# Optimization experiments

Measured on AMD Instinct MI355X. Metric: run time of the kernel, lower is better.

Reference implementation:

```python
import jax, jax.numpy as jnp
import numpy as np

CLAMP = 60.0
EPS = 1e-4

def _make_weights(N, alpha_logits, delta_logits, beta_logits):
    alpha = jax.nn.sigmoid(alpha_logits)   # [C,H]
    delta = jax.nn.sigmoid(delta_logits)
    beta = jax.nn.sigmoid(beta_logits)
    A = alpha * beta                        # [C,H]
    r = jnp.clip(1.0 - alpha * delta, EPS, 1.0 - EPS)
    t = jnp.arange(N, dtype=jnp.float32)[:, None, None]   # [N,1,1]
    logr = jnp.clip(jnp.log(r) * t, -CLAMP, CLAMP)        # [N,C,H]
    return A, jnp.exp(logr), jnp.exp(-logr)

def _ema_fwd(x, A, eta, r_pos, r_neg):
    # x: [B,N,C] -> y: [B,N,C]
    z = A * x[..., None] * r_neg            # [B,N,C,H]
    h = jnp.cumsum(z, axis=1) * r_pos       # [B,N,C,H]
    return jnp.sum(eta * h, axis=-1)        # [B,N,C]

def reference(x, alpha_logits, delta_logits, beta_logits, eta, proj_w, proj_b):
    B, N, C = x.shape
    A, r_pos, r_neg = _make_weights(N, alpha_logits, delta_logits, beta_logits)
    xf = x.astype(jnp.float32)
    y_fwd = _ema_fwd(xf, A, eta, r_pos, r_neg)
    y_bwd = _ema_fwd(xf[:, ::-1], A, eta, r_pos, r_neg)[:, ::-1]
    z = jnp.concatenate([y_fwd, y_bwd], axis=-1).astype(x.dtype)  # [B,N,2C]
    return z @ proj_w.T + proj_b            # [B,N,C]

def setup_inputs():
    key = jax.random.key(0)
    ks = jax.random.split(key, 7)
    B, N, C, H = 8, 4096, 512, 4
    return {
        "x": jax.random.normal(ks[0], (B, N, C), dtype=jnp.float32),
        "alpha_logits": jax.random.normal(ks[1], (C, H), dtype=jnp.float32),
        "delta_logits": jax.random.normal(ks[2], (C, H), dtype=jnp.float32),
        "beta_logits": jax.random.normal(ks[3], (C, H), dtype=jnp.float32),
        "eta": jax.random.normal(ks[4], (C, H), dtype=jnp.float32) * 0.02,
        "proj_w": jax.random.normal(ks[5], (C, 2 * C), dtype=jnp.float32) / np.sqrt(2.0 * C),
        "proj_b": jax.random.normal(ks[6], (C,), dtype=jnp.float32) * 0.01,
    }
```

## Files before the change

kernel.cpp:

```cpp
#include <hip/hip_runtime.h>
#include <hip/hip_bf16.h>

#define B_ 8
#define N_ 4096
#define C_ 512
#define H_ 4
#define EPS_ 1e-4f
#define E60P 1.14200739e26f
#define E60M 8.7565108e-27f

typedef __attribute__((ext_vector_type(8))) short short8;
typedef __attribute__((ext_vector_type(4))) float floatx4;
typedef __attribute__((ext_vector_type(2))) float floatx2;
typedef __attribute__((ext_vector_type(4))) unsigned short ushort4_t;
typedef unsigned short ushort_t;

__device__ __forceinline__ float sigmoidf_(float v) {
    return 1.0f / (1.0f + expf(-v));
}

__device__ __forceinline__ int pk_off(int t, int w, int k0, int ks, int f,
                                      int lane8, int kb) {
    return ((((t * 2 + w) * 16 + k0) * 2 + ks) * 4 + f) * 512 + lane8 * 8 + kb;
}

__device__ __forceinline__ void gload16(const void* g, void* l) {
    __builtin_amdgcn_global_load_lds(
        (const __attribute__((address_space(1))) void*)g,
        (__attribute__((address_space(3))) void*)l, 16, 0, 0);
}

__global__ __launch_bounds__(256) void k_partials3(
    const float* __restrict__ x, const float* __restrict__ al,
    const float* __restrict__ dl, const float* __restrict__ bl,
    float* __restrict__ P)
{
    int bid   = blockIdx.x;
    int chunk = bid & 15;
    int ct    = (bid >> 4) & 7;
    int b     = bid >> 7;
    int lane  = threadIdx.x & 63;
    int wave  = threadIdx.x >> 6;
    int c     = ct * 64 + lane;
    int sub   = chunk * 4 + wave;
    int t0f   = sub * 64;
    int t0b   = (63 - sub) * 64;

    float aa[4], dd[4], bb[4];
    { float4 v = ((const float4*)al)[c]; aa[0]=v.x; aa[1]=v.y; aa[2]=v.z; aa[3]=v.w; }
    { float4 v = ((const float4*)dl)[c]; dd[0]=v.x; dd[1]=v.y; dd[2]=v.z; dd[3]=v.w; }
    { float4 v = ((const float4*)bl)[c]; bb[0]=v.x; bb[1]=v.y; bb[2]=v.z; bb[3]=v.w; }

    float A[H_], ri[H_], Lh[H_];
    #pragma unroll
    for (int h = 0; h < H_; ++h) {
        float alpha = sigmoidf_(aa[h]);
        float delta = sigmoidf_(dd[h]);
        float beta  = sigmoidf_(bb[h]);
        A[h] = alpha * beta;
        float r = fminf(fmaxf(1.0f - alpha * delta, EPS_), 1.0f - EPS_);
        Lh[h] = logf(r);
        ri[h] = 1.0f / r;
    }
    const floatx2 E2P = {E60P, E60P};
    floatx2 A2[2]  = {{A[0],  A[1]},  {A[2],  A[3]}};
    floatx2 ri2[2] = {{ri[0], ri[1]}, {ri[2], ri[3]}};

    const float* xp = x + ((size_t)b * N_ + t0f) * C_ + c;

    floatx2 ep2[2], T2[2];
    #pragma unroll
    for (int p = 0; p < 2; ++p) {
        ep2[p] = (floatx2){expf(fminf(-Lh[2*p]   * (float)t0f, 60.0f)),
                           expf(fminf(-Lh[2*p+1] * (float)t0f, 60.0f))};
        T2[p]  = (floatx2){0.f, 0.f};
    }
    {
        float cur[8];
        #pragma unroll
        for (int j = 0; j < 8; ++j) cur[j] = xp[(size_t)j * C_];
        #pragma unroll 1
        for (int g = 0; g < 8; ++g) {
            float nxt[8];
            if (g < 7) {
                #pragma unroll
                for (int j = 0; j < 8; ++j)
                    nxt[j] = xp[(size_t)(g * 8 + 8 + j) * C_];
            }
            #pragma unroll
            for (int j = 0; j < 8; ++j) {
                floatx2 xv2 = {cur[j], cur[j]};
                #pragma unroll
                for (int p = 0; p < 2; ++p) {
                    T2[p] += (A2[p] * xv2) * ep2[p];
                    ep2[p] = __builtin_elementwise_min(ep2[p] * ri2[p], E2P);
                }
            }
            if (g < 7) {
                #pragma unroll
                for (int j = 0; j < 8; ++j) cur[j] = nxt[j];
            }
        }
        float* pp = P + ((size_t)b * 64 + sub) * (H_ * C_) + c;
        pp[0]      = T2[0].x;  pp[C_]     = T2[0].y;
        pp[2 * C_] = T2[1].x;  pp[3 * C_] = T2[1].y;
    }

    #pragma unroll
    for (int p = 0; p < 2; ++p) {
        ep2[p] = (floatx2){expf(fminf(-Lh[2*p]   * (float)t0b, 60.0f)),
                           expf(fminf(-Lh[2*p+1] * (float)t0b, 60.0f))};
        T2[p]  = (floatx2){0.f, 0.f};
    }
    {
        float cur[8];
        #pragma unroll
        for (int j = 0; j < 8; ++j) cur[j] = xp[(size_t)(63 - j) * C_];
        #pragma unroll 1
        for (int g = 0; g < 8; ++g) {
            float nxt[8];
            if (g < 7) {
                #pragma unroll
                for (int j = 0; j < 8; ++j)
                    nxt[j] = xp[(size_t)(63 - (g * 8 + 8 + j)) * C_];
            }
            #pragma unroll
            for (int j = 0; j < 8; ++j) {
                floatx2 xv2 = {cur[j], cur[j]};
                #pragma unroll
                for (int p = 0; p < 2; ++p) {
                    T2[p] += (A2[p] * xv2) * ep2[p];
                    ep2[p] = __builtin_elementwise_min(ep2[p] * ri2[p], E2P);
                }
            }
            if (g < 7) {
                #pragma unroll
                for (int j = 0; j < 8; ++j) cur[j] = nxt[j];
            }
        }
        float* pp = P + ((size_t)(8 + b) * 64 + (63 - sub)) * (H_ * C_) + c;
        pp[0]      = T2[0].x;  pp[C_]     = T2[0].y;
        pp[2 * C_] = T2[1].x;  pp[3 * C_] = T2[1].y;
    }
}

__global__ __launch_bounds__(256) void k_scan(float* __restrict__ P)
{
    int bid = blockIdx.x;
    int ct  = bid & 7;
    int b   = (bid >> 3) & 7;
    int dir = bid >> 6;
    int cl  = threadIdx.x & 63;
    int h   = threadIdx.x >> 6;
    int c   = ct * 64 + cl;

    float* base = P + ((size_t)(dir * 8 + b) * 64) * (H_ * C_) + h * C_ + c;

    float v[64];
    #pragma unroll
    for (int s = 0; s < 64; ++s) v[s] = base[s * (H_ * C_)];

    float run = 0.0f;
    #pragma unroll
    for (int s = 0; s < 64; ++s) { float t = v[s]; v[s] = run; run += t; }

    #pragma unroll
    for (int s = 0; s < 64; ++s) base[s * (H_ * C_)] = v[s];
}

__global__ __launch_bounds__(256) void k_apply3(
    const float* __restrict__ x, const float* __restrict__ al,
    const float* __restrict__ dl, const float* __restrict__ bl,
    const float* __restrict__ eta, const float* __restrict__ P,
    ushort_t* __restrict__ Zp)
{
    int bid   = blockIdx.x;
    int chunk = bid & 15;
    int ct    = (bid >> 4) & 7;
    int b     = bid >> 7;
    int lane  = threadIdx.x & 63;
    int wave  = threadIdx.x >> 6;
    int c     = ct * 64 + lane;
    int sub   = chunk * 4 + wave;
    int t0f   = sub * 64;
    int t0b   = (63 - sub) * 64;

    int ksv = lane >> 5, qv = (lane >> 3) & 3, kbv = lane & 7;
    int mt  = b * 32 + (t0f >> 7);
    int wq  = (t0f >> 6) & 1;
    int offcF = pk_off(mt, wq, ct,     ksv, 0, qv * 16, kbv);
    int offcB = pk_off(mt, wq, 8 + ct, ksv, 0, qv * 16, kbv);

    float aa[4], dd[4], bb[4], ee[4];
    { float4 v = ((const float4*)al )[c]; aa[0]=v.x; aa[1]=v.y; aa[2]=v.z; aa[3]=v.w; }
    { float4 v = ((const float4*)dl )[c]; dd[0]=v.x; dd[1]=v.y; dd[2]=v.z; dd[3]=v.w; }
    { float4 v = ((const float4*)bl )[c]; bb[0]=v.x; bb[1]=v.y; bb[2]=v.z; bb[3]=v.w; }
    { float4 v = ((const float4*)eta)[c]; ee[0]=v.x; ee[1]=v.y; ee[2]=v.z; ee[3]=v.w; }

    float A[H_], rr[H_], ri[H_], Lh[H_];
    #pragma unroll
    for (int h = 0; h < H_; ++h) {
        float alpha = sigmoidf_(aa[h]);
        float delta = sigmoidf_(dd[h]);
        float beta  = sigmoidf_(bb[h]);
        A[h] = alpha * beta;
        float r = fminf(fmaxf(1.0f - alpha * delta, EPS_), 1.0f - EPS_);
        Lh[h] = logf(r);
        rr[h] = r;
        ri[h] = 1.0f / r;
    }
    const floatx2 E2P = {E60P, E60P};
    const floatx2 E2M = {E60M, E60M};
    floatx2 A2[2]  = {{A[0],  A[1]},  {A[2],  A[3]}};
    floatx2 ri2[2] = {{ri[0], ri[1]}, {ri[2], ri[3]}};
    floatx2 rr2[2] = {{rr[0], rr[1]}, {rr[2], rr[3]}};
    floatx2 ee2[2] = {{ee[0], ee[1]}, {ee[2], ee[3]}};

    const float* xp = x + ((size_t)b * N_ + t0f) * C_ + c;

    {
        const float* cp = P + ((size_t)b * 64 + sub) * (H_ * C_) + c;
        floatx2 ep2[2], em2[2], S2[2];
        #pragma unroll
        for (int p = 0; p < 2; ++p) {
            ep2[p] = (floatx2){expf(fminf(-Lh[2*p]   * (float)t0f, 60.0f)),
                               expf(fminf(-Lh[2*p+1] * (float)t0f, 60.0f))};
            em2[p] = (floatx2){expf(fmaxf( Lh[2*p]   * (float)t0f, -60.0f)),
                               expf(fmaxf( Lh[2*p+1] * (float)t0f, -60.0f))};
            S2[p]  = (floatx2){cp[(2*p) * C_], cp[(2*p+1) * C_]};
        }
        float cur[8];
        #pragma unroll
        for (int j = 0; j < 8; ++j) cur[j] = xp[(size_t)j * C_];
        #pragma unroll 1
        for (int g = 0; g < 8; ++g) {
            float nxt[8];
            if (g < 7) {
                #pragma unroll
                for (int j = 0; j < 8; ++j)
                    nxt[j] = xp[(size_t)(g * 8 + 8 + j) * C_];
            }
            #pragma unroll
            for (int j = 0; j < 8; ++j) {
                int i = g * 8 + j;
                floatx2 xv2 = {cur[j], cur[j]};
                floatx2 acc = {0.f, 0.f};
                #pragma unroll
                for (int p = 0; p < 2; ++p) {
                    S2[p] += (A2[p] * xv2) * ep2[p];
                    ep2[p] = __builtin_elementwise_min(ep2[p] * ri2[p], E2P);
                    acc   += ee2[p] * (em2[p] * S2[p]);
                    em2[p] = __builtin_elementwise_max(em2[p] * rr2[p], E2M);
                }
                float y = acc.x + acc.y;
                __hip_bfloat16 yb = __float2bfloat16(y);
                Zp[offcF + (i >> 4) * 512 + (i & 15) * 8] = *(ushort_t*)&yb;
            }
            if (g < 7) {
                #pragma unroll
                for (int j = 0; j < 8; ++j) cur[j] = nxt[j];
            }
        }
    }

    {
        const float* cp = P + ((size_t)(8 + b) * 64 + (63 - sub)) * (H_ * C_) + c;
        floatx2 ep2[2], em2[2], S2[2];
        #pragma unroll
        for (int p = 0; p < 2; ++p) {
            ep2[p] = (floatx2){expf(fminf(-Lh[2*p]   * (float)t0b, 60.0f)),
                               expf(fminf(-Lh[2*p+1] * (float)t0b, 60.0f))};
            em2[p] = (floatx2){expf(fmaxf( Lh[2*p]   * (float)t0b, -60.0f)),
                               expf(fmaxf( Lh[2*p+1] * (float)t0b, -60.0f))};
            S2[p]  = (floatx2){cp[(2*p) * C_], cp[(2*p+1) * C_]};
        }
        float cur[8];
        #pragma unroll
        for (int j = 0; j < 8; ++j) cur[j] = xp[(size_t)(63 - j) * C_];
        #pragma unroll 1
        for (int g = 0; g < 8; ++g) {
            float nxt[8];
            if (g < 7) {
                #pragma unroll
                for (int j = 0; j < 8; ++j)
                    nxt[j] = xp[(size_t)(63 - (g * 8 + 8 + j)) * C_];
            }
            #pragma unroll
            for (int j = 0; j < 8; ++j) {
                int i = 63 - (g * 8 + j);
                floatx2 xv2 = {cur[j], cur[j]};
                floatx2 acc = {0.f, 0.f};
                #pragma unroll
                for (int p = 0; p < 2; ++p) {
                    S2[p] += (A2[p] * xv2) * ep2[p];
                    ep2[p] = __builtin_elementwise_min(ep2[p] * ri2[p], E2P);
                    acc   += ee2[p] * (em2[p] * S2[p]);
                    em2[p] = __builtin_elementwise_max(em2[p] * rr2[p], E2M);
                }
                float y = acc.x + acc.y;
                __hip_bfloat16 yb = __float2bfloat16(y);
                Zp[offcB + (i >> 4) * 512 + (i & 15) * 8] = *(ushort_t*)&yb;
            }
            if (g < 7) {
                #pragma unroll
                for (int j = 0; j < 8; ++j) cur[j] = nxt[j];
            }
        }
    }
}

__global__ __launch_bounds__(256) void k_cvtw2(const float* __restrict__ w,
                                               ushort_t* __restrict__ Wp)
{
    int i4 = blockIdx.x * 256 + threadIdx.x;
    int i  = i4 << 2;
    int n = i >> 10, k = i & 1023;
    int nt = n >> 7, rn = n & 127;
    int k0 = k >> 6, kk = k & 63;
    int off = pk_off(nt, rn >> 6, k0, kk >> 5, (rn >> 4) & 3,
                     ((kk >> 3) & 3) * 16 + (rn & 15), kk & 7);
    float4 v = ((const float4*)w)[i4];
    ushort4_t r;
    { __hip_bfloat16 t = __float2bfloat16(v.x); r.x = *(ushort_t*)&t; }
    { __hip_bfloat16 t = __float2bfloat16(v.y); r.y = *(ushort_t*)&t; }
    { __hip_bfloat16 t = __float2bfloat16(v.z); r.z = *(ushort_t*)&t; }
    { __hip_bfloat16 t = __float2bfloat16(v.w); r.w = *(ushort_t*)&t; }
    *(ushort4_t*)&Wp[off] = r;
}

__global__ __launch_bounds__(256, 4) void k_gemm3(
    const ushort_t* __restrict__ Zp, const ushort_t* __restrict__ Wp,
    const float* __restrict__ bias, float* __restrict__ out)
{
    __shared__ __align__(16) char lds[32768];
    char*  ldsA = lds;
    char*  ldsB = lds + 16384;
    float* stg  = (float*)lds;

    int tid  = threadIdx.x;
    int lane = tid & 63, wave = tid >> 6;
    int wm   = wave & 1, wn = wave >> 1;
    int fr   = lane & 15, quad = lane >> 4;

    int bid = blockIdx.x;
    int mt  = ((bid >> 5) << 3) | (bid & 7);
    int nt  = (bid >> 3) & 3;
    int m0  = mt * 128, n0 = nt * 128;

    const ushort_t* Az = Zp + ((size_t)(mt * 2) * 16) * 4096;
    const ushort_t* Bz = Wp + ((size_t)(nt * 2) * 16) * 4096;

    floatx4 acc[4][4];
    #pragma unroll
    for (int mf = 0; mf < 4; ++mf)
        #pragma unroll
        for (int nf = 0; nf < 4; ++nf)
            acc[mf][nf] = (floatx4){0.f, 0.f, 0.f, 0.f};

    for (int k0 = 0; k0 < 16; ++k0) {
        const ushort_t* As = Az + (size_t)k0 * 4096;
        const ushort_t* Bs = Bz + (size_t)k0 * 4096;
        #pragma unroll
        for (int w = 0; w < 2; ++w)
            #pragma unroll
            for (int inst = 0; inst < 2; ++inst) {
                gload16(As + w * 65536 + inst * 2048 + tid * 8,
                        ldsA + w * 8192 + inst * 4096 + tid * 16);
                gload16(Bs + w * 65536 + inst * 2048 + tid * 8,
                        ldsB + w * 8192 + inst * 4096 + tid * 16);
            }
        asm volatile("s_waitcnt vmcnt(0)" ::: "memory");
        __syncthreads();

        #pragma unroll
        for (int ks = 0; ks < 2; ++ks) {
            short8 af[4], bf[4];
            #pragma unroll
            for (int f = 0; f < 4; ++f) {
                af[f] = *(const short8*)(ldsA + wm * 8192 + (ks * 4 + f) * 1024 + lane * 16);
                bf[f] = *(const short8*)(ldsB + wn * 8192 + (ks * 4 + f) * 1024 + lane * 16);
            }
            #pragma unroll
            for (int mf = 0; mf < 4; ++mf)
                #pragma unroll
                for (int nf = 0; nf < 4; ++nf)
                    acc[mf][nf] = __builtin_amdgcn_mfma_f32_16x16x32_bf16(
                        af[mf], bf[nf], acc[mf][nf], 0, 0, 0);
        }
        __syncthreads();
    }

    int rrow = tid >> 3;
    int seg  = tid & 7;
    int gcol = n0 + seg * 16;

    #pragma unroll
    for (int ch = 0; ch < 4; ++ch) {
        if ((wave & 1) == (ch >> 1)) {
            int ml = (ch & 1) * 2;
            #pragma unroll
            for (int mi = 0; mi < 2; ++mi) {
                #pragma unroll
                for (int nf = 0; nf < 4; ++nf) {
                    int col = wn * 64 + nf * 16 + fr;
                    #pragma unroll
                    for (int rg = 0; rg < 4; ++rg) {
                        int row = mi * 16 + quad * 4 + rg;
                        stg[row * 132 + col] = acc[ml + mi][nf][rg];
                    }
                }
            }
        }
        __syncthreads();
        {
            int gm = m0 + ch * 32 + rrow;
            const float* s = &stg[rrow * 132 + seg * 16];
            #pragma unroll
            for (int k = 0; k < 4; ++k) {
                float4 v  = *(const float4*)&s[k * 4];
                float4 bv = *(const float4*)&bias[gcol + k * 4];
                v.x += bv.x; v.y += bv.y; v.z += bv.z; v.w += bv.w;
                *(float4*)&out[(size_t)gm * 512 + gcol + k * 4] = v;
            }
        }
        __syncthreads();
    }
}

extern "C" void kernel_launch(void* const* d_in, const int* in_sizes, int n_in,
                              void* d_out, int out_size, void* d_ws, size_t ws_size,
                              hipStream_t stream)
{
    const float* x  = (const float*)d_in[0];
    const float* al = (const float*)d_in[1];
    const float* dl = (const float*)d_in[2];
    const float* bl = (const float*)d_in[3];
    const float* et = (const float*)d_in[4];
    const float* pw = (const float*)d_in[5];
    const float* pb = (const float*)d_in[6];
    float* out = (float*)d_out;

    ushort_t* Zp = (ushort_t*)d_ws;
    float*    P  = (float*)((char*)d_ws + 67108864);
    ushort_t* Wp = (ushort_t*)((char*)d_ws + 75497472);

    hipLaunchKernelGGL(k_cvtw2,     dim3(512),  dim3(256), 0, stream, pw, Wp);
    hipLaunchKernelGGL(k_partials3, dim3(1024), dim3(256), 0, stream, x, al, dl, bl, P);
    hipLaunchKernelGGL(k_scan,      dim3(128),  dim3(256), 0, stream, P);
    hipLaunchKernelGGL(k_apply3,    dim3(1024), dim3(256), 0, stream, x, al, dl, bl, et, P, Zp);
    hipLaunchKernelGGL(k_gemm3,     dim3(1024), dim3(256), 0, stream, Zp, Wp, pb, out);
}
```

Before: 224.8 us.

## Split forward/backward scan directions across blocks and fold A into decay factor

The partials and apply kernels now launch twice as many blocks, with each block handling only the forward or only the backward direction rather than both in sequence. The A coefficient is folded into the running decay factor, with the clamp scaled to A·e^60, which removes one multiply per step. Launch bounds now request 8 waves-per-EU occupancy. This is meant to raise parallelism and occupancy for the memory-bound scans. The cost is recomputing the per-channel sigmoid and log setup in twice as many blocks, and a possible register squeeze from the occupancy hint.

```diff
diff --git a/kernel.cpp b/kernel.cpp
--- a/kernel.cpp
+++ b/kernel.cpp
@@ -30,7 +30,7 @@
         (__attribute__((address_space(3))) void*)l, 16, 0, 0);
 }
 
-__global__ __launch_bounds__(256) void k_partials3(
+__global__ __launch_bounds__(256, 8) void k_partials5(
     const float* __restrict__ x, const float* __restrict__ al,
     const float* __restrict__ dl, const float* __restrict__ bl,
     float* __restrict__ P)
@@ -38,7 +38,8 @@
     int bid   = blockIdx.x;
     int chunk = bid & 15;
     int ct    = (bid >> 4) & 7;
-    int b     = bid >> 7;
+    int b     = (bid >> 7) & 7;
+    int dir   = bid >> 10;
     int lane  = threadIdx.x & 63;
     int wave  = threadIdx.x >> 6;
     int c     = ct * 64 + lane;
@@ -62,20 +63,21 @@
         Lh[h] = logf(r);
         ri[h] = 1.0f / r;
     }
-    const floatx2 E2P = {E60P, E60P};
-    floatx2 A2[2]  = {{A[0],  A[1]},  {A[2],  A[3]}};
-    floatx2 ri2[2] = {{ri[0], ri[1]}, {ri[2], ri[3]}};
+    floatx2 ri2[2]  = {{ri[0], ri[1]}, {ri[2], ri[3]}};
+    floatx2 AEP2[2] = {{A[0] * E60P, A[1] * E60P}, {A[2] * E60P, A[3] * E60P}};
 
     const float* xp = x + ((size_t)b * N_ + t0f) * C_ + c;
 
-    floatx2 ep2[2], T2[2];
+    int   t0   = dir ? t0b : t0f;
+    floatx2 Ae2[2], T2[2];
     #pragma unroll
     for (int p = 0; p < 2; ++p) {
-        ep2[p] = (floatx2){expf(fminf(-Lh[2*p]   * (float)t0f, 60.0f)),
-                           expf(fminf(-Lh[2*p+1] * (float)t0f, 60.0f))};
+        Ae2[p] = (floatx2){A[2*p]   * expf(fminf(-Lh[2*p]   * (float)t0, 60.0f)),
+                           A[2*p+1] * expf(fminf(-Lh[2*p+1] * (float)t0, 60.0f))};
         T2[p]  = (floatx2){0.f, 0.f};
     }
-    {
+
+    if (dir == 0) {
         float cur[8];
         #pragma unroll
         for (int j = 0; j < 8; ++j) cur[j] = xp[(size_t)j * C_];
@@ -92,8 +94,8 @@
                 floatx2 xv2 = {cur[j], cur[j]};
                 #pragma unroll
                 for (int p = 0; p < 2; ++p) {
-                    T2[p] += (A2[p] * xv2) * ep2[p];
-                    ep2[p] = __builtin_elementwise_min(ep2[p] * ri2[p], E2P);
+                    T2[p] += Ae2[p] * xv2;
+                    Ae2[p] = __builtin_elementwise_min(Ae2[p] * ri2[p], AEP2[p]);
                 }
             }
             if (g < 7) {
@@ -104,15 +106,7 @@
         float* pp = P + ((size_t)b * 64 + sub) * (H_ * C_) + c;
         pp[0]      = T2[0].x;  pp[C_]     = T2[0].y;
         pp[2 * C_] = T2[1].x;  pp[3 * C_] = T2[1].y;
-    }
-
-    #pragma unroll
-    for (int p = 0; p < 2; ++p) {
-        ep2[p] = (floatx2){expf(fminf(-Lh[2*p]   * (float)t0b, 60.0f)),
-                           expf(fminf(-Lh[2*p+1] * (float)t0b, 60.0f))};
-        T2[p]  = (floatx2){0.f, 0.f};
-    }
-    {
+    } else {
         float cur[8];
         #pragma unroll
         for (int j = 0; j < 8; ++j) cur[j] = xp[(size_t)(63 - j) * C_];
@@ -129,8 +123,8 @@
                 floatx2 xv2 = {cur[j], cur[j]};
                 #pragma unroll
                 for (int p = 0; p < 2; ++p) {
-                    T2[p] += (A2[p] * xv2) * ep2[p];
-                    ep2[p] = __builtin_elementwise_min(ep2[p] * ri2[p], E2P);
+                    T2[p] += Ae2[p] * xv2;
+                    Ae2[p] = __builtin_elementwise_min(Ae2[p] * ri2[p], AEP2[p]);
                 }
             }
             if (g < 7) {
@@ -168,7 +162,7 @@
     for (int s = 0; s < 64; ++s) base[s * (H_ * C_)] = v[s];
 }
 
-__global__ __launch_bounds__(256) void k_apply3(
+__global__ __launch_bounds__(256, 8) void k_apply5(
     const float* __restrict__ x, const float* __restrict__ al,
     const float* __restrict__ dl, const float* __restrict__ bl,
     const float* __restrict__ eta, const float* __restrict__ P,
@@ -177,7 +171,8 @@
     int bid   = blockIdx.x;
     int chunk = bid & 15;
     int ct    = (bid >> 4) & 7;
-    int b     = bid >> 7;
+    int b     = (bid >> 7) & 7;
+    int dir   = bid >> 10;
     int lane  = threadIdx.x & 63;
     int wave  = threadIdx.x >> 6;
     int c     = ct * 64 + lane;
@@ -188,8 +183,6 @@
     int ksv = lane >> 5, qv = (lane >> 3) & 3, kbv = lane & 7;
     int mt  = b * 32 + (t0f >> 7);
     int wq  = (t0f >> 6) & 1;
-    int offcF = pk_off(mt, wq, ct,     ksv, 0, qv * 16, kbv);
-    int offcB = pk_off(mt, wq, 8 + ct, ksv, 0, qv * 16, kbv);
 
     float aa[4], dd[4], bb[4], ee[4];
     { float4 v = ((const float4*)al )[c]; aa[0]=v.x; aa[1]=v.y; aa[2]=v.z; aa[3]=v.w; }
@@ -209,22 +202,22 @@
         rr[h] = r;
         ri[h] = 1.0f / r;
     }
-    const floatx2 E2P = {E60P, E60P};
     const floatx2 E2M = {E60M, E60M};
-    floatx2 A2[2]  = {{A[0],  A[1]},  {A[2],  A[3]}};
-    floatx2 ri2[2] = {{ri[0], ri[1]}, {ri[2], ri[3]}};
-    floatx2 rr2[2] = {{rr[0], rr[1]}, {rr[2], rr[3]}};
-    floatx2 ee2[2] = {{ee[0], ee[1]}, {ee[2], ee[3]}};
+    floatx2 ri2[2]  = {{ri[0], ri[1]}, {ri[2], ri[3]}};
+    floatx2 rr2[2]  = {{rr[0], rr[1]}, {rr[2], rr[3]}};
+    floatx2 ee2[2]  = {{ee[0], ee[1]}, {ee[2], ee[3]}};
+    floatx2 AEP2[2] = {{A[0] * E60P, A[1] * E60P}, {A[2] * E60P, A[3] * E60P}};
 
     const float* xp = x + ((size_t)b * N_ + t0f) * C_ + c;
 
-    {
+    if (dir == 0) {
+        int offcF = pk_off(mt, wq, ct, ksv, 0, qv * 16, kbv);
         const float* cp = P + ((size_t)b * 64 + sub) * (H_ * C_) + c;
-        floatx2 ep2[2], em2[2], S2[2];
+        floatx2 Ae2[2], em2[2], S2[2];
         #pragma unroll
         for (int p = 0; p < 2; ++p) {
-            ep2[p] = (floatx2){expf(fminf(-Lh[2*p]   * (float)t0f, 60.0f)),
-                               expf(fminf(-Lh[2*p+1] * (float)t0f, 60.0f))};
+            Ae2[p] = (floatx2){A[2*p]   * expf(fminf(-Lh[2*p]   * (float)t0f, 60.0f)),
+                               A[2*p+1] * expf(fminf(-Lh[2*p+1] * (float)t0f, 60.0f))};
             em2[p] = (floatx2){expf(fmaxf( Lh[2*p]   * (float)t0f, -60.0f)),
                                expf(fmaxf( Lh[2*p+1] * (float)t0f, -60.0f))};
             S2[p]  = (floatx2){cp[(2*p) * C_], cp[(2*p+1) * C_]};
@@ -247,8 +240,8 @@
                 floatx2 acc = {0.f, 0.f};
                 #pragma unroll
                 for (int p = 0; p < 2; ++p) {
-                    S2[p] += (A2[p] * xv2) * ep2[p];
-                    ep2[p] = __builtin_elementwise_min(ep2[p] * ri2[p], E2P);
+                    S2[p] += Ae2[p] * xv2;
+                    Ae2[p] = __builtin_elementwise_min(Ae2[p] * ri2[p], AEP2[p]);
                     acc   += ee2[p] * (em2[p] * S2[p]);
                     em2[p] = __builtin_elementwise_max(em2[p] * rr2[p], E2M);
                 }
@@ -261,15 +254,14 @@
                 for (int j = 0; j < 8; ++j) cur[j] = nxt[j];
             }
         }
-    }
-
-    {
+    } else {
+        int offcB = pk_off(mt, wq, 8 + ct, ksv, 0, qv * 16, kbv);
         const float* cp = P + ((size_t)(8 + b) * 64 + (63 - sub)) * (H_ * C_) + c;
-        floatx2 ep2[2], em2[2], S2[2];
+        floatx2 Ae2[2], em2[2], S2[2];
         #pragma unroll
         for (int p = 0; p < 2; ++p) {
-            ep2[p] = (floatx2){expf(fminf(-Lh[2*p]   * (float)t0b, 60.0f)),
-                               expf(fminf(-Lh[2*p+1] * (float)t0b, 60.0f))};
+            Ae2[p] = (floatx2){A[2*p]   * expf(fminf(-Lh[2*p]   * (float)t0b, 60.0f)),
+                               A[2*p+1] * expf(fminf(-Lh[2*p+1] * (float)t0b, 60.0f))};
             em2[p] = (floatx2){expf(fmaxf( Lh[2*p]   * (float)t0b, -60.0f)),
                                expf(fmaxf( Lh[2*p+1] * (float)t0b, -60.0f))};
             S2[p]  = (floatx2){cp[(2*p) * C_], cp[(2*p+1) * C_]};
@@ -292,8 +284,8 @@
                 floatx2 acc = {0.f, 0.f};
                 #pragma unroll
                 for (int p = 0; p < 2; ++p) {
-                    S2[p] += (A2[p] * xv2) * ep2[p];
-                    ep2[p] = __builtin_elementwise_min(ep2[p] * ri2[p], E2P);
+                    S2[p] += Ae2[p] * xv2;
+                    Ae2[p] = __builtin_elementwise_min(Ae2[p] * ri2[p], AEP2[p]);
                     acc   += ee2[p] * (em2[p] * S2[p]);
                     em2[p] = __builtin_elementwise_max(em2[p] * rr2[p], E2M);
                 }
@@ -445,8 +437,8 @@
     ushort_t* Wp = (ushort_t*)((char*)d_ws + 75497472);
 
     hipLaunchKernelGGL(k_cvtw2,     dim3(512),  dim3(256), 0, stream, pw, Wp);
-    hipLaunchKernelGGL(k_partials3, dim3(1024), dim3(256), 0, stream, x, al, dl, bl, P);
+    hipLaunchKernelGGL(k_partials5, dim3(2048), dim3(256), 0, stream, x, al, dl, bl, P);
     hipLaunchKernelGGL(k_scan,      dim3(128),  dim3(256), 0, stream, P);
-    hipLaunchKernelGGL(k_apply3,    dim3(1024), dim3(256), 0, stream, x, al, dl, bl, et, P, Zp);
+    hipLaunchKernelGGL(k_apply5,    dim3(2048), dim3(256), 0, stream, x, al, dl, bl, et, P, Zp);
     hipLaunchKernelGGL(k_gemm3,     dim3(1024), dim3(256), 0, stream, Zp, Wp, pb, out);
 }
```

Measured after the change: 220.6 us. About the same (-1.9%).
